# Performance work log

Hardware: AMD Instinct MI355X
Metric: run time of the kernel (lower is better)

Reference implementation:

```python
import jax, jax.numpy as jnp
import numpy as np

B, NX, NC, C, H = 4, 1024, 2048, 1024, 16
DH = C // H            # head_dim = 64
SCALE = DH ** -0.5


def setup_inputs() -> dict:
    key = jax.random.key(0)
    ks = jax.random.split(key, 6)
    # sorted unique token indices to update per batch (== positions where update_mask==1)
    rng = np.random.default_rng(0)
    idx = np.stack([np.sort(rng.permutation(NC)[:NX]) for _ in range(B)]).astype(np.int32)
    return {
        "x": jax.random.normal(ks[0], (B, NX, C), jnp.float32),
        "update_idx": jnp.asarray(idx),                              # (B, NX) int32
        "cache_k": jax.random.normal(ks[1], (B, H, NC, DH), jnp.float32),
        "cache_v": jax.random.normal(ks[2], (B, H, NC, DH), jnp.float32),
        "w_qkv": jax.random.normal(ks[3], (3 * C, C), jnp.float32) * 0.02,
        "b_qkv": jnp.zeros((3 * C,), jnp.float32),
        "w_proj": jax.random.normal(ks[4], (C, C), jnp.float32) * 0.02,
        "b_proj": jnp.zeros((C,), jnp.float32),
    }


def reference(x, update_idx, cache_k, cache_v, w_qkv, b_qkv, w_proj, b_proj):
    Bq, N, Cq = x.shape
    # QKV projection: (B, N, 3C) -> (3, B, H, N, Dh) layout as in torch permute(2,0,3,1,4)
    qkv = (x @ w_qkv.T + b_qkv).reshape(Bq, N, 3, H, DH)
    q = qkv[:, :, 0].transpose(0, 2, 1, 3)  # (B, H, N, Dh)
    k = qkv[:, :, 1].transpose(0, 2, 1, 3)
    v = qkv[:, :, 2].transpose(0, 2, 1, 3)
    # masked_scatter_ of k/v into cache at the masked (updated) token slots.
    # Indices are sorted, so row-order masked_scatter == indexed scatter.
    scat = jax.vmap(lambda cache, idx, src: cache.at[:, idx, :].set(src))
    k_full = scat(cache_k, update_idx, k)    # (B, H, NC, Dh)
    v_full = scat(cache_v, update_idx, v)
    # plain attention: q scaled, full softmax over cache length
    attn = jax.nn.softmax(jnp.einsum('bhqd,bhkd->bhqk', q * SCALE, k_full), axis=-1)
    out = jnp.einsum('bhqk,bhkd->bhqd', attn, v_full)  # (B, H, N, Dh)
    out = out.transpose(0, 2, 1, 3).reshape(Bq, N, Cq)
    return out @ w_proj.T + b_proj
```

## Files before the change

### kernel.cpp

```cpp
#include <hip/hip_runtime.h>
#include <hip/hip_bf16.h>

#define B_   4
#define NX_  1024
#define NC_  2048
#define C_   1024
#define H_   16
#define DH_  64

typedef __attribute__((ext_vector_type(8))) __bf16 bf16x8;
typedef __attribute__((ext_vector_type(4))) float  f32x4;

static __device__ __forceinline__ unsigned short f2bf(float f) {
    unsigned int u = __float_as_uint(f);
    u += 0x7fffu + ((u >> 16) & 1u);
    return (unsigned short)(u >> 16);
}

static __device__ __forceinline__ unsigned int pk2(float lo, float hi) {
    unsigned int a = __float_as_uint(lo) + 0x8000u;
    unsigned int b = __float_as_uint(hi) + 0x8000u;
    return __builtin_amdgcn_perm(b, a, 0x07060302);
}

static __device__ __forceinline__ bf16x8 ldfrag(const unsigned short* p) {
    union { uint4 u; bf16x8 b; } cv;
    cv.u = *reinterpret_cast<const uint4*>(p);
    return cv.b;
}

static __device__ __forceinline__ void gl_lds(const unsigned short* g, unsigned short* l) {
    __builtin_amdgcn_global_load_lds((const __attribute__((address_space(1))) void*)g,
                                     (__attribute__((address_space(3))) void*)l, 16, 0, 0);
}

__global__ __launch_bounds__(256) void cvt_all_kernel(
    const float* __restrict__ x,  const float* __restrict__ wq,
    const float* __restrict__ wp, const float* __restrict__ ck,
    unsigned short* __restrict__ xbf,  unsigned short* __restrict__ wqbf,
    unsigned short* __restrict__ wpbf, unsigned short* __restrict__ kfb) {
    int blk = blockIdx.x;
    const float* src; unsigned short* dst; int i;
    if (blk < 4096)      { src = x;  dst = xbf;  i = blk; }
    else if (blk < 7168) { src = wq; dst = wqbf; i = blk - 4096; }
    else if (blk < 8192) { src = wp; dst = wpbf; i = blk - 7168; }
    else                 { src = ck; dst = kfb;  i = blk - 8192; }
    int idx = i * 256 + threadIdx.x;
    float4 f = reinterpret_cast<const float4*>(src)[idx];
    ushort4 o;
    o.x = f2bf(f.x); o.y = f2bf(f.y); o.z = f2bf(f.z); o.w = f2bf(f.w);
    reinterpret_cast<ushort4*>(dst)[idx] = o;
}

__global__ __launch_bounds__(256) void vt_cvt_kernel(const float* __restrict__ cv_,
                                                     unsigned short* __restrict__ vt) {
    int t   = threadIdx.x;
    int blk = blockIdx.x;
    int bh  = blk >> 6;
    int kg  = blk & 63;
    int d   = t & 63;
    int kci = t >> 6;
    int kc  = kg * 4 + kci;
    const float* src = cv_ + ((size_t)bh * NC_ + (size_t)kc * 8) * DH_ + d;
    union { uint4 u; unsigned short s[8]; } o;
#pragma unroll
    for (int j = 0; j < 8; j++) o.s[j] = f2bf(src[(size_t)j * DH_]);
    *reinterpret_cast<uint4*>(vt + ((size_t)bh * DH_ + d) * NC_ + (size_t)kc * 8) = o.u;
}

static __device__ __forceinline__ void stage32(const unsigned short* g, unsigned short* lds,
                                               int w, int l) {
#pragma unroll
    for (int i = 0; i < 2; i++) {
        const unsigned short* gp = g + (size_t)(w * 32 + i * 16 + (l >> 2)) * C_ + (l & 3) * 8;
        unsigned short* lp = lds + (w * 32 + i * 16) * 32;
        gl_lds(gp, lp);
    }
}

static __device__ __forceinline__ void gemm_core(const unsigned short* Ag, const unsigned short* Bg,
                                                 unsigned short* As, unsigned short* Bs,
                                                 int w, int l, int wr, int wc, int quad, int col,
                                                 f32x4 acc[4][4]) {
    for (int kk = 0; kk < C_; kk += 32) {
        __syncthreads();
        stage32(Ag + kk, As, w, l);
        stage32(Bg + kk, Bs, w, l);
        __syncthreads();
        bf16x8 af[4], bfr[4];
#pragma unroll
        for (int t = 0; t < 4; t++) af[t]  = ldfrag(&As[(wr * 64 + t * 16 + col) * 32 + quad * 8]);
#pragma unroll
        for (int t = 0; t < 4; t++) bfr[t] = ldfrag(&Bs[(wc * 64 + t * 16 + col) * 32 + quad * 8]);
#pragma unroll
        for (int mt = 0; mt < 4; mt++)
#pragma unroll
            for (int nt = 0; nt < 4; nt++)
                acc[mt][nt] = __builtin_amdgcn_mfma_f32_16x16x32_bf16(af[mt], bfr[nt], acc[mt][nt], 0, 0, 0);
    }
}

__global__ __launch_bounds__(256) void qkv_gemm_kernel(
    const unsigned short* __restrict__ xbf,
    const unsigned short* __restrict__ wbf,
    const float* __restrict__ bias,
    const int* __restrict__ uidx,
    unsigned short* __restrict__ qb,
    unsigned short* __restrict__ kf,
    unsigned short* __restrict__ vt)
{
    __shared__ unsigned short As[128 * 32], Bs[128 * 32];
    int bn = blockIdx.x, bm = blockIdx.y;
    int w = threadIdx.x >> 6, l = threadIdx.x & 63;
    int quad = l >> 4, col = l & 15;
    int wr = w >> 1, wc = w & 1;
    f32x4 acc[4][4];
#pragma unroll
    for (int a = 0; a < 4; a++)
#pragma unroll
        for (int b = 0; b < 4; b++) acc[a][b] = (f32x4){0.f, 0.f, 0.f, 0.f};

    gemm_core(xbf + (size_t)(bm * 128) * C_, wbf + (size_t)(bn * 128) * C_,
              As, Bs, w, l, wr, wc, quad, col, acc);

    int part = bn >> 3;
    float bv[4]; int nl[4];
#pragma unroll
    for (int nt = 0; nt < 4; nt++) {
        int n = bn * 128 + wc * 64 + nt * 16 + col;
        bv[nt] = bias[n];
        nl[nt] = n & 1023;
    }
    const float QS = 0.18033688011112042f;
#pragma unroll
    for (int mt = 0; mt < 4; mt++)
#pragma unroll
        for (int r = 0; r < 4; r++) {
            int m = bm * 128 + wr * 64 + mt * 16 + quad * 4 + r;
            int b = m >> 10, i = m & 1023;
            int j = (part == 0) ? 0 : uidx[(b << 10) + i];
#pragma unroll
            for (int nt = 0; nt < 4; nt++) {
                int h = nl[nt] >> 6, d = nl[nt] & 63;
                float v = acc[mt][nt][r] + bv[nt];
                if (part == 0)
                    qb[((size_t)(b * H_ + h) * NX_ + i) * DH_ + d] = f2bf(v * QS);
                else if (part == 1)
                    kf[((size_t)(b * H_ + h) * NC_ + j) * DH_ + d] = f2bf(v);
                else
                    vt[((size_t)(b * H_ + h) * DH_ + d) * NC_ + j] = f2bf(v);
            }
        }
}

#define PST 40
__global__ __launch_bounds__(256, 4) void attn_kernel(
    const unsigned short* __restrict__ qb,
    const unsigned short* __restrict__ kf,
    const unsigned short* __restrict__ vt,
    unsigned short* __restrict__ ao)
{
    __shared__ unsigned short Klo[64 * 32], Khi[64 * 32];
    __shared__ unsigned short V0s[64 * 32], V1s[64 * 32];
    __shared__ unsigned short Psh[4][16 * PST];
    int id = blockIdx.x;
    int qt = (id >> 3) & 15;
    int bh = ((id >> 7) << 3) | (id & 7);
    int wave = threadIdx.x >> 6, lane = threadIdx.x & 63;
    int quad = lane >> 4, col = lane & 15;
    int srow = lane >> 2, schk = lane & 3;

    const unsigned short* qrow = qb + ((size_t)bh * NX_ + qt * 64 + wave * 16 + col) * DH_;
    bf16x8 qf0 = ldfrag(qrow + quad * 8);
    bf16x8 qf1 = ldfrag(qrow + 32 + quad * 8);

    const unsigned short* kbase = kf + (size_t)bh * NC_ * DH_;
    const unsigned short* vbase = vt + (size_t)bh * DH_ * NC_;
    unsigned short* Pw = &Psh[wave][0];

    f32x4 o[4];
#pragma unroll
    for (int t = 0; t < 4; t++) o[t] = (f32x4){0.f, 0.f, 0.f, 0.f};
    float l_i = 0.f;

    for (int kb = 0; kb < 32; kb++) {
        __syncthreads();
        {
            const unsigned short* Kt = kbase + (size_t)(kb * 64 + wave * 16 + srow) * DH_;
            gl_lds(Kt +      schk * 8, Klo + wave * 16 * 32);
            gl_lds(Kt + 32 + schk * 8, Khi + wave * 16 * 32);
            const unsigned short* Vt = vbase + (size_t)(wave * 16 + srow) * NC_ + kb * 64;
            gl_lds(Vt +      schk * 8, V0s + wave * 16 * 32);
            gl_lds(Vt + 32 + schk * 8, V1s + wave * 16 * 32);
        }
        __syncthreads();

#pragma unroll
        for (int ks = 0; ks < 2; ks++) {
            f32x4 s0 = (f32x4){0.f, 0.f, 0.f, 0.f};
            f32x4 s1 = (f32x4){0.f, 0.f, 0.f, 0.f};
            {
                bf16x8 a0 = ldfrag(&Klo[(ks * 32 +      col) * 32 + quad * 8]);
                bf16x8 b0 = ldfrag(&Khi[(ks * 32 +      col) * 32 + quad * 8]);
                bf16x8 a1 = ldfrag(&Klo[(ks * 32 + 16 + col) * 32 + quad * 8]);
                bf16x8 b1 = ldfrag(&Khi[(ks * 32 + 16 + col) * 32 + quad * 8]);
                s0 = __builtin_amdgcn_mfma_f32_16x16x32_bf16(a0, qf0, s0, 0, 0, 0);
                s0 = __builtin_amdgcn_mfma_f32_16x16x32_bf16(b0, qf1, s0, 0, 0, 0);
                s1 = __builtin_amdgcn_mfma_f32_16x16x32_bf16(a1, qf0, s1, 0, 0, 0);
                s1 = __builtin_amdgcn_mfma_f32_16x16x32_bf16(b1, qf1, s1, 0, 0, 0);
            }
            const unsigned short* Vs = (ks == 0) ? V0s : V1s;
            bf16x8 vfr[4];
#pragma unroll
            for (int t = 0; t < 4; t++) vfr[t] = ldfrag(&Vs[(t * 16 + col) * 32 + quad * 8]);
            {
                float p0 = exp2f(s0[0]), p1 = exp2f(s0[1]), p2 = exp2f(s0[2]), p3 = exp2f(s0[3]);
                float p4 = exp2f(s1[0]), p5 = exp2f(s1[1]), p6 = exp2f(s1[2]), p7 = exp2f(s1[3]);
                l_i += ((p0 + p1) + (p2 + p3)) + ((p4 + p5) + (p6 + p7));
                uint2 w0; w0.x = pk2(p0, p1); w0.y = pk2(p2, p3);
                uint2 w1; w1.x = pk2(p4, p5); w1.y = pk2(p6, p7);
                *reinterpret_cast<uint2*>(&Pw[col * PST +      quad * 4]) = w0;
                *reinterpret_cast<uint2*>(&Pw[col * PST + 16 + quad * 4]) = w1;
            }
            asm volatile("" ::: "memory");
            {
                bf16x8 pf = ldfrag(&Pw[col * PST + quad * 8]);
#pragma unroll
                for (int t = 0; t < 4; t++)
                    o[t] = __builtin_amdgcn_mfma_f32_16x16x32_bf16(vfr[t], pf, o[t], 0, 0, 0);
            }
            asm volatile("" ::: "memory");
        }
    }

    l_i += __shfl_xor(l_i, 16, 64);
    l_i += __shfl_xor(l_i, 32, 64);
    float inv = 1.f / l_i;

    int b = bh >> 4, h = bh & 15;
    int q = qt * 64 + wave * 16 + col;
    unsigned short* orow = ao + ((size_t)b * NX_ + q) * C_ + h * 64;
#pragma unroll
    for (int t = 0; t < 4; t++) {
        uint2 ov;
        ov.x = pk2(o[t][0] * inv, o[t][1] * inv);
        ov.y = pk2(o[t][2] * inv, o[t][3] * inv);
        *reinterpret_cast<uint2*>(&orow[t * 16 + quad * 4]) = ov;
    }
}

__global__ __launch_bounds__(256) void proj_gemm_kernel(
    const unsigned short* __restrict__ abf,
    const unsigned short* __restrict__ wbf,
    const float* __restrict__ bias,
    float* __restrict__ out)
{
    __shared__ unsigned short As[128 * 32], Bs[128 * 32];
    int bn = blockIdx.x, bm = blockIdx.y;
    int w = threadIdx.x >> 6, l = threadIdx.x & 63;
    int quad = l >> 4, col = l & 15;
    int wr = w >> 1, wc = w & 1;
    f32x4 acc[4][4];
#pragma unroll
    for (int a = 0; a < 4; a++)
#pragma unroll
        for (int b = 0; b < 4; b++) acc[a][b] = (f32x4){0.f, 0.f, 0.f, 0.f};

    gemm_core(abf + (size_t)(bm * 128) * C_, wbf + (size_t)(bn * 128) * C_,
              As, Bs, w, l, wr, wc, quad, col, acc);

    float bv[4];
#pragma unroll
    for (int nt = 0; nt < 4; nt++) bv[nt] = bias[bn * 128 + wc * 64 + nt * 16 + col];
#pragma unroll
    for (int mt = 0; mt < 4; mt++)
#pragma unroll
        for (int r = 0; r < 4; r++) {
            int m = bm * 128 + wr * 64 + mt * 16 + quad * 4 + r;
#pragma unroll
            for (int nt = 0; nt < 4; nt++) {
                int n = bn * 128 + wc * 64 + nt * 16 + col;
                out[(size_t)m * C_ + n] = acc[mt][nt][r] + bv[nt];
            }
        }
}

extern "C" void kernel_launch(void* const* d_in, const int* in_sizes, int n_in,
                              void* d_out, int out_size, void* d_ws, size_t ws_size,
                              hipStream_t stream) {
    const float* x      = (const float*)d_in[0];
    const int*   uidx   = (const int*)  d_in[1];
    const float* cachek = (const float*)d_in[2];
    const float* cachev = (const float*)d_in[3];
    const float* wqkv   = (const float*)d_in[4];
    const float* bqkv   = (const float*)d_in[5];
    const float* wproj  = (const float*)d_in[6];
    const float* bproj  = (const float*)d_in[7];
    float* out = (float*)d_out;

    char* ws = (char*)d_ws;
    unsigned short* xbf  = (unsigned short*)(ws);
    unsigned short* wqbf = (unsigned short*)(ws + (8ull  << 20));
    unsigned short* wpbf = (unsigned short*)(ws + (14ull << 20));
    unsigned short* qb   = (unsigned short*)(ws + (16ull << 20));
    unsigned short* kfb  = (unsigned short*)(ws + (24ull << 20));
    unsigned short* vtb  = (unsigned short*)(ws + (40ull << 20));
    unsigned short* aob  = (unsigned short*)(ws + (56ull << 20));

    cvt_all_kernel<<<16384, 256, 0, stream>>>(x, wqkv, wproj, cachek, xbf, wqbf, wpbf, kfb);
    vt_cvt_kernel <<<4096, 256, 0, stream>>>(cachev, vtb);

    qkv_gemm_kernel <<<dim3(24, 32), 256, 0, stream>>>(xbf, wqbf, bqkv, uidx, qb, kfb, vtb);
    attn_kernel     <<<1024, 256, 0, stream>>>(qb, kfb, vtb, aob);
    proj_gemm_kernel<<<dim3(8, 32),  256, 0, stream>>>(aob, wpbf, bproj, out);
}
```

Baseline: 282.4 us.

## Register-prefetch LDS pipelining with padded tiles; fuse convert kernels; retile proj GEMM

Replaces the direct global-to-LDS loads in the QKV GEMM, attention and projection kernels with a register-staged prefetch. The next tile is loaded into registers while the current one is computed, then written into LDS tiles padded to a row stride of 40 to avoid bank conflicts. The two fp32-to-bf16 conversion kernels are merged into one launch. The projection GEMM moves to 128x64 tiles to double its grid. In exchange the kernels use more registers, and the launch bounds now hint at 3 blocks per SM for the GEMMs.

```diff
diff --git a/kernel.cpp b/kernel.cpp
--- a/kernel.cpp
+++ b/kernel.cpp
@@ -29,78 +29,44 @@
     return cv.b;
 }
 
-static __device__ __forceinline__ void gl_lds(const unsigned short* g, unsigned short* l) {
-    __builtin_amdgcn_global_load_lds((const __attribute__((address_space(1))) void*)g,
-                                     (__attribute__((address_space(3))) void*)l, 16, 0, 0);
-}
-
 __global__ __launch_bounds__(256) void cvt_all_kernel(
     const float* __restrict__ x,  const float* __restrict__ wq,
     const float* __restrict__ wp, const float* __restrict__ ck,
+    const float* __restrict__ cv_,
     unsigned short* __restrict__ xbf,  unsigned short* __restrict__ wqbf,
-    unsigned short* __restrict__ wpbf, unsigned short* __restrict__ kfb) {
+    unsigned short* __restrict__ wpbf, unsigned short* __restrict__ kfb,
+    unsigned short* __restrict__ vt) {
     int blk = blockIdx.x;
-    const float* src; unsigned short* dst; int i;
-    if (blk < 4096)      { src = x;  dst = xbf;  i = blk; }
-    else if (blk < 7168) { src = wq; dst = wqbf; i = blk - 4096; }
-    else if (blk < 8192) { src = wp; dst = wpbf; i = blk - 7168; }
-    else                 { src = ck; dst = kfb;  i = blk - 8192; }
-    int idx = i * 256 + threadIdx.x;
-    float4 f = reinterpret_cast<const float4*>(src)[idx];
-    ushort4 o;
-    o.x = f2bf(f.x); o.y = f2bf(f.y); o.z = f2bf(f.z); o.w = f2bf(f.w);
-    reinterpret_cast<ushort4*>(dst)[idx] = o;
-}
-
-__global__ __launch_bounds__(256) void vt_cvt_kernel(const float* __restrict__ cv_,
-                                                     unsigned short* __restrict__ vt) {
-    int t   = threadIdx.x;
-    int blk = blockIdx.x;
-    int bh  = blk >> 6;
-    int kg  = blk & 63;
-    int d   = t & 63;
-    int kci = t >> 6;
-    int kc  = kg * 4 + kci;
-    const float* src = cv_ + ((size_t)bh * NC_ + (size_t)kc * 8) * DH_ + d;
-    union { uint4 u; unsigned short s[8]; } o;
-#pragma unroll
-    for (int j = 0; j < 8; j++) o.s[j] = f2bf(src[(size_t)j * DH_]);
-    *reinterpret_cast<uint4*>(vt + ((size_t)bh * DH_ + d) * NC_ + (size_t)kc * 8) = o.u;
-}
-
-static __device__ __forceinline__ void stage32(const unsigned short* g, unsigned short* lds,
-                                               int w, int l) {
-#pragma unroll
-    for (int i = 0; i < 2; i++) {
-        const unsigned short* gp = g + (size_t)(w * 32 + i * 16 + (l >> 2)) * C_ + (l & 3) * 8;
-        unsigned short* lp = lds + (w * 32 + i * 16) * 32;
-        gl_lds(gp, lp);
-    }
-}
-
-static __device__ __forceinline__ void gemm_core(const unsigned short* Ag, const unsigned short* Bg,
-                                                 unsigned short* As, unsigned short* Bs,
-                                                 int w, int l, int wr, int wc, int quad, int col,
-                                                 f32x4 acc[4][4]) {
-    for (int kk = 0; kk < C_; kk += 32) {
-        __syncthreads();
-        stage32(Ag + kk, As, w, l);
-        stage32(Bg + kk, Bs, w, l);
-        __syncthreads();
-        bf16x8 af[4], bfr[4];
-#pragma unroll
-        for (int t = 0; t < 4; t++) af[t]  = ldfrag(&As[(wr * 64 + t * 16 + col) * 32 + quad * 8]);
-#pragma unroll
-        for (int t = 0; t < 4; t++) bfr[t] = ldfrag(&Bs[(wc * 64 + t * 16 + col) * 32 + quad * 8]);
-#pragma unroll
-        for (int mt = 0; mt < 4; mt++)
-#pragma unroll
-            for (int nt = 0; nt < 4; nt++)
-                acc[mt][nt] = __builtin_amdgcn_mfma_f32_16x16x32_bf16(af[mt], bfr[nt], acc[mt][nt], 0, 0, 0);
-    }
-}
-
-__global__ __launch_bounds__(256) void qkv_gemm_kernel(
+    if (blk < 16384) {
+        const float* src; unsigned short* dst; int i;
+        if (blk < 4096)      { src = x;  dst = xbf;  i = blk; }
+        else if (blk < 7168) { src = wq; dst = wqbf; i = blk - 4096; }
+        else if (blk < 8192) { src = wp; dst = wpbf; i = blk - 7168; }
+        else                 { src = ck; dst = kfb;  i = blk - 8192; }
+        int idx = i * 256 + threadIdx.x;
+        float4 f = reinterpret_cast<const float4*>(src)[idx];
+        ushort4 o;
+        o.x = f2bf(f.x); o.y = f2bf(f.y); o.z = f2bf(f.z); o.w = f2bf(f.w);
+        reinterpret_cast<ushort4*>(dst)[idx] = o;
+    } else {
+        int i   = blk - 16384;
+        int t   = threadIdx.x;
+        int bh  = i >> 6;
+        int kg  = i & 63;
+        int d   = t & 63;
+        int kci = t >> 6;
+        int kc  = kg * 4 + kci;
+        const float* src = cv_ + ((size_t)bh * NC_ + (size_t)kc * 8) * DH_ + d;
+        union { uint4 u; unsigned short s[8]; } o;
+#pragma unroll
+        for (int j = 0; j < 8; j++) o.s[j] = f2bf(src[(size_t)j * DH_]);
+        *reinterpret_cast<uint4*>(vt + ((size_t)bh * DH_ + d) * NC_ + (size_t)kc * 8) = o.u;
+    }
+}
+
+#define LSTR 40
+
+__global__ __launch_bounds__(256, 3) void qkv_gemm_kernel(
     const unsigned short* __restrict__ xbf,
     const unsigned short* __restrict__ wbf,
     const float* __restrict__ bias,
@@ -109,19 +75,64 @@
     unsigned short* __restrict__ kf,
     unsigned short* __restrict__ vt)
 {
-    __shared__ unsigned short As[128 * 32], Bs[128 * 32];
+    __shared__ unsigned short As[128 * LSTR], Bs[128 * LSTR];
     int bn = blockIdx.x, bm = blockIdx.y;
     int w = threadIdx.x >> 6, l = threadIdx.x & 63;
     int quad = l >> 4, col = l & 15;
     int wr = w >> 1, wc = w & 1;
+    int srow = w * 32 + (l >> 2), schk = (l & 3) * 8;
+
+    const unsigned short* Ap = xbf + (size_t)(bm * 128 + srow) * C_ + schk;
+    const unsigned short* Bp = wbf + (size_t)(bn * 128 + srow) * C_ + schk;
+    unsigned short* Aw = As + srow * LSTR + schk;
+    unsigned short* Bw = Bs + srow * LSTR + schk;
+
     f32x4 acc[4][4];
 #pragma unroll
     for (int a = 0; a < 4; a++)
 #pragma unroll
         for (int b = 0; b < 4; b++) acc[a][b] = (f32x4){0.f, 0.f, 0.f, 0.f};
 
-    gemm_core(xbf + (size_t)(bm * 128) * C_, wbf + (size_t)(bn * 128) * C_,
-              As, Bs, w, l, wr, wc, quad, col, acc);
+    uint4 ar0, ar1, br0, br1;
+#define LDREG(kk_)                                                       \
+    {   int kk = (kk_) * 32;                                             \
+        ar0 = *reinterpret_cast<const uint4*>(Ap + kk);                  \
+        ar1 = *reinterpret_cast<const uint4*>(Ap + 16 * C_ + kk);        \
+        br0 = *reinterpret_cast<const uint4*>(Bp + kk);                  \
+        br1 = *reinterpret_cast<const uint4*>(Bp + 16 * C_ + kk);        \
+    }
+#define WRTILE()                                                         \
+    {   *reinterpret_cast<uint4*>(Aw)             = ar0;                 \
+        *reinterpret_cast<uint4*>(Aw + 16 * LSTR) = ar1;                 \
+        *reinterpret_cast<uint4*>(Bw)             = br0;                 \
+        *reinterpret_cast<uint4*>(Bw + 16 * LSTR) = br1;                 \
+    }
+
+    LDREG(0);
+    WRTILE();
+    LDREG(1);
+    __syncthreads();
+#pragma unroll 1
+    for (int it = 0; it < 32; it++) {
+        bf16x8 af[4], bfr[4];
+#pragma unroll
+        for (int t = 0; t < 4; t++) af[t]  = ldfrag(&As[(wr * 64 + t * 16 + col) * LSTR + quad * 8]);
+#pragma unroll
+        for (int t = 0; t < 4; t++) bfr[t] = ldfrag(&Bs[(wc * 64 + t * 16 + col) * LSTR + quad * 8]);
+#pragma unroll
+        for (int mt = 0; mt < 4; mt++)
+#pragma unroll
+            for (int nt = 0; nt < 4; nt++)
+                acc[mt][nt] = __builtin_amdgcn_mfma_f32_16x16x32_bf16(af[mt], bfr[nt], acc[mt][nt], 0, 0, 0);
+        if (it < 31) {
+            __syncthreads();
+            WRTILE();
+            LDREG(it + 2 < 31 ? it + 2 : 31);
+            __syncthreads();
+        }
+    }
+#undef LDREG
+#undef WRTILE
 
     int part = bn >> 3;
     float bv[4]; int nl[4];
@@ -160,22 +171,26 @@
     const unsigned short* __restrict__ vt,
     unsigned short* __restrict__ ao)
 {
-    __shared__ unsigned short Klo[64 * 32], Khi[64 * 32];
-    __shared__ unsigned short V0s[64 * 32], V1s[64 * 32];
+    __shared__ unsigned short Klo[64 * LSTR], Khi[64 * LSTR];
+    __shared__ unsigned short V0s[64 * LSTR], V1s[64 * LSTR];
     __shared__ unsigned short Psh[4][16 * PST];
     int id = blockIdx.x;
     int qt = (id >> 3) & 15;
     int bh = ((id >> 7) << 3) | (id & 7);
     int wave = threadIdx.x >> 6, lane = threadIdx.x & 63;
     int quad = lane >> 4, col = lane & 15;
-    int srow = lane >> 2, schk = lane & 3;
+    int srow = wave * 16 + (lane >> 2), schk = (lane & 3) * 8;
 
     const unsigned short* qrow = qb + ((size_t)bh * NX_ + qt * 64 + wave * 16 + col) * DH_;
     bf16x8 qf0 = ldfrag(qrow + quad * 8);
     bf16x8 qf1 = ldfrag(qrow + 32 + quad * 8);
 
-    const unsigned short* kbase = kf + (size_t)bh * NC_ * DH_;
-    const unsigned short* vbase = vt + (size_t)bh * DH_ * NC_;
+    const unsigned short* Kp = kf + ((size_t)bh * NC_ + srow) * DH_ + schk;
+    const unsigned short* Vp = vt + ((size_t)bh * DH_ + srow) * NC_ + schk;
+    unsigned short* Kwl = Klo + srow * LSTR + schk;
+    unsigned short* Kwh = Khi + srow * LSTR + schk;
+    unsigned short* Vw0 = V0s + srow * LSTR + schk;
+    unsigned short* Vw1 = V1s + srow * LSTR + schk;
     unsigned short* Pw = &Psh[wave][0];
 
     f32x4 o[4];
@@ -183,27 +198,36 @@
     for (int t = 0; t < 4; t++) o[t] = (f32x4){0.f, 0.f, 0.f, 0.f};
     float l_i = 0.f;
 
+    uint4 kr0, kr1, vr0, vr1;
+#define LDREG(kb_)                                                        \
+    {   kr0 = *reinterpret_cast<const uint4*>(Kp + (size_t)(kb_) * 64 * DH_);      \
+        kr1 = *reinterpret_cast<const uint4*>(Kp + (size_t)(kb_) * 64 * DH_ + 32); \
+        vr0 = *reinterpret_cast<const uint4*>(Vp + (kb_) * 64);           \
+        vr1 = *reinterpret_cast<const uint4*>(Vp + (kb_) * 64 + 32);      \
+    }
+#define WRTILE()                                                          \
+    {   *reinterpret_cast<uint4*>(Kwl) = kr0;                             \
+        *reinterpret_cast<uint4*>(Kwh) = kr1;                             \
+        *reinterpret_cast<uint4*>(Vw0) = vr0;                             \
+        *reinterpret_cast<uint4*>(Vw1) = vr1;                             \
+    }
+
+    LDREG(0);
+    WRTILE();
+    LDREG(1);
+    __syncthreads();
+
+#pragma unroll 1
     for (int kb = 0; kb < 32; kb++) {
-        __syncthreads();
-        {
-            const unsigned short* Kt = kbase + (size_t)(kb * 64 + wave * 16 + srow) * DH_;
-            gl_lds(Kt +      schk * 8, Klo + wave * 16 * 32);
-            gl_lds(Kt + 32 + schk * 8, Khi + wave * 16 * 32);
-            const unsigned short* Vt = vbase + (size_t)(wave * 16 + srow) * NC_ + kb * 64;
-            gl_lds(Vt +      schk * 8, V0s + wave * 16 * 32);
-            gl_lds(Vt + 32 + schk * 8, V1s + wave * 16 * 32);
-        }
-        __syncthreads();
-
 #pragma unroll
         for (int ks = 0; ks < 2; ks++) {
             f32x4 s0 = (f32x4){0.f, 0.f, 0.f, 0.f};
             f32x4 s1 = (f32x4){0.f, 0.f, 0.f, 0.f};
             {
-                bf16x8 a0 = ldfrag(&Klo[(ks * 32 +      col) * 32 + quad * 8]);
-                bf16x8 b0 = ldfrag(&Khi[(ks * 32 +      col) * 32 + quad * 8]);
-                bf16x8 a1 = ldfrag(&Klo[(ks * 32 + 16 + col) * 32 + quad * 8]);
-                bf16x8 b1 = ldfrag(&Khi[(ks * 32 + 16 + col) * 32 + quad * 8]);
+                bf16x8 a0 = ldfrag(&Klo[(ks * 32 +      col) * LSTR + quad * 8]);
+                bf16x8 b0 = ldfrag(&Khi[(ks * 32 +      col) * LSTR + quad * 8]);
+                bf16x8 a1 = ldfrag(&Klo[(ks * 32 + 16 + col) * LSTR + quad * 8]);
+                bf16x8 b1 = ldfrag(&Khi[(ks * 32 + 16 + col) * LSTR + quad * 8]);
                 s0 = __builtin_amdgcn_mfma_f32_16x16x32_bf16(a0, qf0, s0, 0, 0, 0);
                 s0 = __builtin_amdgcn_mfma_f32_16x16x32_bf16(b0, qf1, s0, 0, 0, 0);
                 s1 = __builtin_amdgcn_mfma_f32_16x16x32_bf16(a1, qf0, s1, 0, 0, 0);
@@ -212,7 +236,7 @@
             const unsigned short* Vs = (ks == 0) ? V0s : V1s;
             bf16x8 vfr[4];
 #pragma unroll
-            for (int t = 0; t < 4; t++) vfr[t] = ldfrag(&Vs[(t * 16 + col) * 32 + quad * 8]);
+            for (int t = 0; t < 4; t++) vfr[t] = ldfrag(&Vs[(t * 16 + col) * LSTR + quad * 8]);
             {
                 float p0 = exp2f(s0[0]), p1 = exp2f(s0[1]), p2 = exp2f(s0[2]), p3 = exp2f(s0[3]);
                 float p4 = exp2f(s1[0]), p5 = exp2f(s1[1]), p6 = exp2f(s1[2]), p7 = exp2f(s1[3]);
@@ -231,7 +255,15 @@
             }
             asm volatile("" ::: "memory");
         }
-    }
+        if (kb < 31) {
+            __syncthreads();
+            WRTILE();
+            LDREG(kb + 2 < 31 ? kb + 2 : 31);
+            __syncthreads();
+        }
+    }
+#undef LDREG
+#undef WRTILE
 
     l_i += __shfl_xor(l_i, 16, 64);
     l_i += __shfl_xor(l_i, 32, 64);
@@ -249,37 +281,79 @@
     }
 }
 
-__global__ __launch_bounds__(256) void proj_gemm_kernel(
+__global__ __launch_bounds__(256, 3) void proj_gemm_kernel(
     const unsigned short* __restrict__ abf,
     const unsigned short* __restrict__ wbf,
     const float* __restrict__ bias,
     float* __restrict__ out)
 {
-    __shared__ unsigned short As[128 * 32], Bs[128 * 32];
+    __shared__ unsigned short As[128 * LSTR], Bs[64 * LSTR];
     int bn = blockIdx.x, bm = blockIdx.y;
     int w = threadIdx.x >> 6, l = threadIdx.x & 63;
     int quad = l >> 4, col = l & 15;
-    int wr = w >> 1, wc = w & 1;
-    f32x4 acc[4][4];
-#pragma unroll
-    for (int a = 0; a < 4; a++)
+    int sarow = w * 32 + (l >> 2), sbrow = w * 16 + (l >> 2), schk = (l & 3) * 8;
+
+    const unsigned short* Ap = abf + (size_t)(bm * 128 + sarow) * C_ + schk;
+    const unsigned short* Bp = wbf + (size_t)(bn * 64 + sbrow) * C_ + schk;
+    unsigned short* Aw = As + sarow * LSTR + schk;
+    unsigned short* Bw = Bs + sbrow * LSTR + schk;
+
+    f32x4 acc[2][4];
+#pragma unroll
+    for (int a = 0; a < 2; a++)
 #pragma unroll
         for (int b = 0; b < 4; b++) acc[a][b] = (f32x4){0.f, 0.f, 0.f, 0.f};
 
-    gemm_core(abf + (size_t)(bm * 128) * C_, wbf + (size_t)(bn * 128) * C_,
-              As, Bs, w, l, wr, wc, quad, col, acc);
+    uint4 ar0, ar1, br0;
+#define LDREG(kk_)                                                       \
+    {   int kk = (kk_) * 32;                                             \
+        ar0 = *reinterpret_cast<const uint4*>(Ap + kk);                  \
+        ar1 = *reinterpret_cast<const uint4*>(Ap + 16 * C_ + kk);        \
+        br0 = *reinterpret_cast<const uint4*>(Bp + kk);                  \
+    }
+#define WRTILE()                                                         \
+    {   *reinterpret_cast<uint4*>(Aw)             = ar0;                 \
+        *reinterpret_cast<uint4*>(Aw + 16 * LSTR) = ar1;                 \
+        *reinterpret_cast<uint4*>(Bw)             = br0;                 \
+    }
+
+    LDREG(0);
+    WRTILE();
+    LDREG(1);
+    __syncthreads();
+#pragma unroll 1
+    for (int it = 0; it < 32; it++) {
+        bf16x8 af[2], bfr[4];
+#pragma unroll
+        for (int t = 0; t < 2; t++) af[t]  = ldfrag(&As[(w * 32 + t * 16 + col) * LSTR + quad * 8]);
+#pragma unroll
+        for (int t = 0; t < 4; t++) bfr[t] = ldfrag(&Bs[(t * 16 + col) * LSTR + quad * 8]);
+#pragma unroll
+        for (int mt = 0; mt < 2; mt++)
+#pragma unroll
+            for (int nt = 0; nt < 4; nt++)
+                acc[mt][nt] = __builtin_amdgcn_mfma_f32_16x16x32_bf16(af[mt], bfr[nt], acc[mt][nt], 0, 0, 0);
+        if (it < 31) {
+            __syncthreads();
+            WRTILE();
+            LDREG(it + 2 < 31 ? it + 2 : 31);
+            __syncthreads();
+        }
+    }
+#undef LDREG
+#undef WRTILE
 
     float bv[4];
 #pragma unroll
-    for (int nt = 0; nt < 4; nt++) bv[nt] = bias[bn * 128 + wc * 64 + nt * 16 + col];
-#pragma unroll
-    for (int mt = 0; mt < 4; mt++)
+    for (int nt = 0; nt < 4; nt++) bv[nt] = bias[bn * 64 + nt * 16 + col];
+#pragma unroll
+    for (int mt = 0; mt < 2; mt++)
 #pragma unroll
         for (int r = 0; r < 4; r++) {
-            int m = bm * 128 + wr * 64 + mt * 16 + quad * 4 + r;
+            int m = bm * 128 + w * 32 + mt * 16 + quad * 4 + r;
 #pragma unroll
             for (int nt = 0; nt < 4; nt++) {
-                int n = bn * 128 + wc * 64 + nt * 16 + col;
+                int n = bn * 64 + nt * 16 + col;
                 out[(size_t)m * C_ + n] = acc[mt][nt][r] + bv[nt];
             }
         }
@@ -307,10 +381,9 @@
     unsigned short* vtb  = (unsigned short*)(ws + (40ull << 20));
     unsigned short* aob  = (unsigned short*)(ws + (56ull << 20));
 
-    cvt_all_kernel<<<16384, 256, 0, stream>>>(x, wqkv, wproj, cachek, xbf, wqbf, wpbf, kfb);
-    vt_cvt_kernel <<<4096, 256, 0, stream>>>(cachev, vtb);
-
+    cvt_all_kernel<<<20480, 256, 0, stream>>>(x, wqkv, wproj, cachek, cachev,
+                                              xbf, wqbf, wpbf, kfb, vtb);
     qkv_gemm_kernel <<<dim3(24, 32), 256, 0, stream>>>(xbf, wqbf, bqkv, uidx, qb, kfb, vtb);
     attn_kernel     <<<1024, 256, 0, stream>>>(qb, kfb, vtb, aob);
-    proj_gemm_kernel<<<dim3(8, 32),  256, 0, stream>>>(aob, wpbf, bproj, out);
-}
+    proj_gemm_kernel<<<dim3(16, 32), 256, 0, stream>>>(aob, wpbf, bproj, out);
+}
```

New measurement: 272.2 us. 1.04x faster.
